# Optimization experiments

Measured on AMD Instinct MI355X. Metric: run time of the kernel, lower is better.

The kernel has to match this reference:

```python
import jax, jax.numpy as jnp
import numpy as np

B, S, D, H = 2, 2048, 2048, 16
HD = D // H  # 128


def setup_inputs() -> dict:
    key = jax.random.key(0)
    ks = jax.random.split(key, 6)
    sc = 0.02
    return {
        "x": jax.random.normal(ks[0], (B, S, D), jnp.float32),
        "attention_mask": jnp.ones((B, S), jnp.int32),
        "w_qkv": jax.random.normal(ks[1], (D, 3 * D), jnp.float32) * sc,
        "b_qkv": jnp.zeros((3 * D,), jnp.float32),
        "w_o": jax.random.normal(ks[2], (D, D), jnp.float32) * sc,
        "b_o": jnp.zeros((D,), jnp.float32),
        "ln1_w": jnp.ones((D,), jnp.float32),
        "w1": jax.random.normal(ks[3], (D, 8 * D), jnp.float32) * sc,
        "b1": jnp.zeros((8 * D,), jnp.float32),
        "w2": jax.random.normal(ks[4], (4 * D, D), jnp.float32) * sc,
        "b2": jnp.zeros((D,), jnp.float32),
        "ln2_w": jnp.ones((D,), jnp.float32),
    }


def rmsnorm(x, w, eps=1e-6):
    rms = jnp.sqrt(jnp.mean(x * x, axis=-1, keepdims=True) + eps)
    return w * (x / rms)


def rope_tables(seq_len, dim, base=10000.0):
    inv_freq = 1.0 / (base ** (jnp.arange(0, dim, 2, dtype=jnp.float32) / dim))
    t = jnp.arange(seq_len, dtype=jnp.float32)
    freqs = t[:, None] * inv_freq[None, :]          # [S, dim/2]
    emb = jnp.concatenate([freqs, freqs], axis=-1)  # [S, dim]
    return jnp.cos(emb), jnp.sin(emb)


def apply_rope(x, cos, sin):
    # Faithful to source: rotate pairs, then out = rot*cos + roll(rot,1)*sin
    xr = x.reshape(*x.shape[:-1], -1, 2)
    x1, x2 = xr[..., 0], xr[..., 1]
    rot = jnp.stack([-x2, x1], axis=-1).reshape(x.shape)
    return rot * cos + jnp.roll(rot, shift=1, axis=-1) * sin


def transformer_layer(x, attention_mask, w_qkv, b_qkv, w_o, b_o, ln1_w, w1, b1, w2, b2, ln2_w):
    residual = x
    qkv = x @ w_qkv + b_qkv                         # [B,S,3D]
    q, k, v = jnp.split(qkv, 3, axis=-1)
    split = lambda t: t.reshape(B, S, H, HD).transpose(0, 2, 1, 3)  # [B,H,S,HD]
    q, k, v = split(q), split(k), split(v)

    cos, sin = rope_tables(S, HD)                   # [S,HD], broadcasts over B,H
    q = apply_rope(q, cos, sin)
    k = apply_rope(k, cos, sin)

    scores = jnp.einsum("bhqd,bhkd->bhqk", q, k) / jnp.sqrt(jnp.float32(HD))
    mask = (attention_mask == 1)[:, None, None, :]  # [B,1,1,S]
    scores = jnp.where(mask, scores, -jnp.inf)
    attn = jax.nn.softmax(scores, axis=-1)
    out = jnp.einsum("bhqk,bhkd->bhqd", attn, v)
    out = out.transpose(0, 2, 1, 3).reshape(B, S, D)
    out = out @ w_o + b_o

    x = rmsnorm(out + residual, ln1_w)
    residual = x
    h = x @ w1 + b1                                 # [B,S,8D]
    h, gate = jnp.split(h, 2, axis=-1)
    h = h * jax.nn.gelu(gate, approximate=False)
    h = h @ w2 + b2
    return rmsnorm(h + residual, ln2_w)


def reference(x, attention_mask, w_qkv, b_qkv, w_o, b_o, ln1_w, w1, b1, w2, b2, ln2_w):
    return transformer_layer(x, attention_mask, w_qkv, b_qkv, w_o, b_o, ln1_w, w1, b1, w2, b2, ln2_w)
```

## Files before the change

### kernel.cpp

```cpp
#include <hip/hip_runtime.h>
#include <cstdint>
#include <cstring>

typedef unsigned short u16;
typedef __attribute__((ext_vector_type(8))) short short8;
typedef __attribute__((ext_vector_type(8))) unsigned short ushortx8;
typedef __attribute__((ext_vector_type(4))) float floatx4;

#define DEV __device__ __forceinline__

DEV u16 f2bf(float f) {
  union { float f; uint32_t u; } x; x.f = f;
  uint32_t r = x.u + 0x7fffu + ((x.u >> 16) & 1u);
  return (u16)(r >> 16);
}
DEV float bf2f(u16 h) {
  union { float f; uint32_t u; } x; x.u = ((uint32_t)h) << 16;
  return x.f;
}
DEV u16 f2h(float f) {
  union { u16 u; _Float16 h; } x; x.h = (_Float16)f; return x.u;
}
DEV float h2f(u16 h) {
  union { u16 u; _Float16 h; } x; x.u = h; return (float)x.h;
}
DEV float fexp2(float x) { return __builtin_amdgcn_exp2f(x); }
DEV float fast_gelu(float g) {
  float u = 0.7978845608f * (g + 0.044715f * g * g * g);
  float e = fexp2(-2.885390082f * fabsf(u));
  float th = (1.0f - e) / (1.0f + e);
  th = (u < 0.0f) ? -th : th;
  return 0.5f * g * (1.0f + th);
}
DEV void gload_lds16(const void* g, void* lds) {
  __builtin_amdgcn_global_load_lds(
      (const __attribute__((address_space(1))) char*)(uintptr_t)g,
      (__attribute__((address_space(3))) char*)(uintptr_t)lds, 16, 0, 0);
}


__global__ __launch_bounds__(256) void k_cvt_bf16(const float* __restrict__ in,
                                                  u16* __restrict__ out, int n) {
  int i = (blockIdx.x * 256 + threadIdx.x) * 8;
  if (i + 7 < n) {
    float4 a = *(const float4*)(in + i);
    float4 b = *(const float4*)(in + i + 4);
    ushortx8 o;
    o[0] = f2bf(a.x); o[1] = f2bf(a.y); o[2] = f2bf(a.z); o[3] = f2bf(a.w);
    o[4] = f2bf(b.x); o[5] = f2bf(b.y); o[6] = f2bf(b.z); o[7] = f2bf(b.w);
    *(ushortx8*)(out + i) = o;
  }
}

__global__ __launch_bounds__(256) void k_transpose_all(const float* __restrict__ Wq,
                                                       u16* __restrict__ WqT,
                                                       const float* __restrict__ Wo,
                                                       u16* __restrict__ WoT,
                                                       const float* __restrict__ W2,
                                                       u16* __restrict__ W2T) {
  __shared__ u16 t[64][70];
  int id = blockIdx.x;
  const float* W; u16* Wt; int R, C, tix;
  if (id < 3072)      { W = Wq; Wt = WqT; R = 2048; C = 6144; tix = id; }
  else if (id < 4096) { W = Wo; Wt = WoT; R = 2048; C = 2048; tix = id - 3072; }
  else                { W = W2; Wt = W2T; R = 8192; C = 2048; tix = id - 4096; }
  int ntc = C >> 6;
  int c0 = (tix % ntc) * 64, r0 = (tix / ntc) * 64;
  int cx = threadIdx.x & 15, ry = threadIdx.x >> 4;
#pragma unroll
  for (int i = 0; i < 4; ++i) {
    int row = ry + i * 16;
    float4 v = *(const float4*)(W + (size_t)(r0 + row) * C + c0 + cx * 4);
    ushort2 lo, hi;
    lo.x = f2bf(v.x); lo.y = f2bf(v.y);
    hi.x = f2bf(v.z); hi.y = f2bf(v.w);
    *(ushort2*)&t[row][cx * 4] = lo;
    *(ushort2*)&t[row][cx * 4 + 2] = hi;
  }
  __syncthreads();
#pragma unroll
  for (int i = 0; i < 4; ++i) {
    int col = ry + i * 16;
    ushort4 o;
    o.x = t[cx * 4 + 0][col]; o.y = t[cx * 4 + 1][col];
    o.z = t[cx * 4 + 2][col]; o.w = t[cx * 4 + 3][col];
    *(ushort4*)(Wt + (size_t)(c0 + col) * R + r0 + cx * 4) = o;
  }
}

__global__ __launch_bounds__(256) void k_transpose_w1p(const float* __restrict__ W,
                                                       u16* __restrict__ Wt) {
  __shared__ u16 t[64][70];
  int c0 = blockIdx.x * 64;
  int r0 = blockIdx.y * 64;
  int cx = threadIdx.x & 15, ry = threadIdx.x >> 4;
  int eta = c0 + cx * 4;
  int Bq = eta >> 8, ii = eta & 255, wn = (ii >> 6) & 3, rr = ii & 63, n = rr >> 4, tt = rr & 15;
  int src = Bq * 128 + wn * 32 + (n & 1) * 16 + tt + ((n >= 2) ? 8192 : 0);
#pragma unroll
  for (int i = 0; i < 4; ++i) {
    int row = ry + i * 16;
    float4 v = *(const float4*)(W + (size_t)(r0 + row) * 16384 + src);
    ushort2 lo, hi;
    lo.x = f2bf(v.x); lo.y = f2bf(v.y);
    hi.x = f2bf(v.z); hi.y = f2bf(v.w);
    *(ushort2*)&t[row][cx * 4] = lo;
    *(ushort2*)&t[row][cx * 4 + 2] = hi;
  }
  __syncthreads();
#pragma unroll
  for (int i = 0; i < 4; ++i) {
    ushort4 o;
    int col = ry + i * 16;
    o.x = t[cx * 4 + 0][col]; o.y = t[cx * 4 + 1][col];
    o.z = t[cx * 4 + 2][col]; o.w = t[cx * 4 + 3][col];
    *(ushort4*)(Wt + (size_t)(c0 + col) * 2048 + r0 + cx * 4) = o;
  }
}

__global__ __launch_bounds__(256) void k_rope_tab(float* __restrict__ ct, float* __restrict__ st) {
  int i = blockIdx.x * 256 + threadIdx.x;
  int s = i >> 6, j = i & 63;
  float invf = 1.0f / powf(10000.0f, (float)j * (1.0f / 64.0f));
  float ang = (float)s * invf;
  ct[i] = cosf(ang);
  st[i] = sinf(ang);
}

template <int EPI>
__global__ __launch_bounds__(512, 2) void k_gemm256(const u16* __restrict__ A,
                                                    const u16* __restrict__ Bt,
                                                    void* __restrict__ C,
                                                    const float* __restrict__ bias,
                                                    int M, int N, int K, int nsplit,
                                                    u16* __restrict__ qrO,
                                                    u16* __restrict__ krO,
                                                    u16* __restrict__ vtO,
                                                    const float* __restrict__ ctabO,
                                                    const float* __restrict__ stabO) {
  __shared__ __align__(16) u16 lds[4][2][8192];
  const int tid = threadIdx.x;
  const int w = tid >> 6, lane = tid & 63;
  const int l15 = lane & 15, l4 = lane >> 4;
  const int wm = w >> 2, wn = w & 3;
  const int nbn = N >> 8;
  const int nbm = M >> 8;

  int bm, bn, split = 0;
  if (nsplit == 1 && nbm == 16 && (nbn & 7) == 0) {
    const int xcd = blockIdx.x & 7, l = blockIdx.x >> 3;
    const int xr = xcd >> 1, xc = xcd & 1;
    const int stn = l >> 4, lbm = (l >> 2) & 3, lbn = l & 3;
    bm = xr * 4 + lbm;
    bn = xc * (nbn >> 1) + stn * 4 + lbn;
  } else {
    const int nwg = gridDim.x;
    const int q = nwg >> 3, r8 = nwg & 7;
    const int xcd = blockIdx.x & 7, loc = blockIdx.x >> 3;
    const int swz = (xcd < r8 ? xcd * (q + 1) : r8 * (q + 1) + (xcd - r8) * q) + loc;
    const int ntiles = nwg / nsplit;
    split = swz / ntiles;
    const int tix = swz % ntiles;
    bm = tix / nbn; bn = tix % nbn;
  }
  const int klen = K / nsplit;
  const int kofs = split * klen;

  const size_t abase = (size_t)bm * 256 * K + kofs;
  const size_t bbase = (size_t)bn * 256 * K + kofs;
  const int nt = klen >> 5;

  const int sr = tid >> 2;
  const int sc = (tid & 3) ^ ((sr >> 1) & 3);
  auto stage = [&](int kt, int li, int op) {
    const u16* src = op ? (Bt + bbase) : (A + abase);
    gload_lds16(src + (size_t)(li * 128 + sr) * K + kt * 32 + sc * 8,
                (void*)&lds[kt & 3][op][(li * 512 + w * 64) * 8]);
  };

  const int fro = l15 * 32 + (l4 ^ ((l15 >> 1) & 3)) * 8;

  floatx4 acc[8][4];
  floatx4 zero = {0.f, 0.f, 0.f, 0.f};
#pragma unroll
  for (int m = 0; m < 8; ++m)
#pragma unroll
    for (int n = 0; n < 4; ++n) acc[m][n] = zero;

  for (int kt = 0; kt < 3; ++kt)
    if (kt < nt) {
      stage(kt, 0, 0); stage(kt, 0, 1);
      stage(kt, 1, 0); stage(kt, 1, 1);
    }

  for (int t = 0; t < nt; ++t) {
    const int buf = t & 3;
    if (t < nt - 2)       asm volatile("s_waitcnt vmcnt(8)" ::: "memory");
    else if (t == nt - 2) asm volatile("s_waitcnt vmcnt(4)" ::: "memory");
    else                  asm volatile("s_waitcnt vmcnt(0)" ::: "memory");
    __builtin_amdgcn_sched_barrier(0);
    __builtin_amdgcn_s_barrier();
    const u16* Ab = &lds[buf][0][wm * 4096 + fro];
    const u16* Bb = &lds[buf][1][wn * 2048 + fro];
    short8 av[4], bv[4];
#pragma unroll
    for (int n = 0; n < 4; ++n) bv[n] = *(const short8*)(Bb + n * 512);
#pragma unroll
    for (int i = 0; i < 4; ++i) av[i] = *(const short8*)(Ab + i * 512);
    if (t + 3 < nt) { stage(t + 3, 0, 0); stage(t + 3, 0, 1); }
    asm volatile("s_waitcnt lgkmcnt(0)" ::: "memory");
    __builtin_amdgcn_sched_barrier(0);
    __builtin_amdgcn_s_setprio(1);
#pragma unroll
    for (int i = 0; i < 4; ++i)
#pragma unroll
      for (int n = 0; n < 4; ++n)
        acc[i][n] = __builtin_amdgcn_mfma_f32_16x16x32_bf16(av[i], bv[n], acc[i][n], 0, 0, 0);
    __builtin_amdgcn_s_setprio(0);
    __builtin_amdgcn_s_barrier();
#pragma unroll
    for (int i = 0; i < 4; ++i) av[i] = *(const short8*)(Ab + (4 + i) * 512);
    if (t + 3 < nt) { stage(t + 3, 1, 0); stage(t + 3, 1, 1); }
    asm volatile("s_waitcnt lgkmcnt(0)" ::: "memory");
    __builtin_amdgcn_sched_barrier(0);
    __builtin_amdgcn_s_setprio(1);
#pragma unroll
    for (int i = 0; i < 4; ++i)
#pragma unroll
      for (int n = 0; n < 4; ++n)
        acc[4 + i][n] = __builtin_amdgcn_mfma_f32_16x16x32_bf16(av[i], bv[n], acc[4 + i][n], 0, 0, 0);
    __builtin_amdgcn_s_setprio(0);
  }

  const int row0 = bm * 256 + wm * 128, col0 = bn * 256 + wn * 64;
  if (EPI == 2) {
    u16* P = (u16*)C + (size_t)split * M * N;
#pragma unroll
    for (int n = 0; n < 4; ++n) {
      int col = col0 + n * 16 + l15;
#pragma unroll
      for (int m = 0; m < 8; ++m)
#pragma unroll
        for (int j = 0; j < 4; ++j) {
          int row = row0 + m * 16 + l4 * 4 + j;
          P[(size_t)row * N + col] = f2h(acc[m][n][j]);
        }
    }
  } else if (EPI == 3) {
    __syncthreads();
    u16* ep = ((u16*)lds) + w * 4096;
    const int colA = bn * 128 + wn * 32;
#pragma unroll
    for (int n = 0; n < 2; ++n) {
      float ba = bias[colA + n * 16 + l15];
      float bg = bias[8192 + colA + n * 16 + l15];
#pragma unroll
      for (int m = 0; m < 8; ++m)
#pragma unroll
        for (int j = 0; j < 4; ++j) {
          float a = acc[m][n][j] + ba;
          float g = acc[m][n + 2][j] + bg;
          ep[(m * 16 + l4 * 4 + j) * 32 + n * 16 + l15] = f2bf(a * fast_gelu(g));
        }
    }
    const int rr = lane >> 2, cg = lane & 3;
    u16* Cg = (u16*)C;
    const int Nact = N >> 1;
#pragma unroll
    for (int pass = 0; pass < 8; ++pass) {
      short8 v = *(const short8*)&ep[(pass * 16 + rr) * 32 + cg * 8];
      size_t grow = row0 + pass * 16 + rr;
      *(short8*)&Cg[grow * Nact + colA + cg * 8] = v;
    }
  } else if (EPI == 4) {
    constexpr int PAD = 264;
    u16* T = (u16*)lds;
    const int bq = bm >> 3;
    const int srow0 = (bm & 7) * 256;
#pragma unroll 1
    for (int hf = 0; hf < 2; ++hf) {
      __syncthreads();
      if (wm == hf) {
#pragma unroll
        for (int n = 0; n < 4; ++n) {
          float bb = bias[bn * 256 + wn * 64 + n * 16 + l15];
#pragma unroll
          for (int m = 0; m < 8; ++m)
#pragma unroll
            for (int j = 0; j < 4; ++j)
              T[(m * 16 + l4 * 4 + j) * PAD + wn * 64 + n * 16 + l15] =
                  f2bf(acc[m][n][j] + bb);
        }
      }
      __syncthreads();
      if (bn < 16) {
        int sl = tid >> 2, hh = (tid >> 1) & 1, t2 = tid & 1;
        const u16* row = T + sl * PAD + hh * 128;
        int s = srow0 + hf * 128 + sl;
        int head = 2 * (bn & 7) + hh;
        u16* dst = (bn < 8 ? qrO : krO) +
                   (((size_t)bq * 16 + head) * 2048 + s) * 128 + t2 * 64;
        const float* ctr = ctabO + (s << 6);
        const float* str2 = stabO + (s << 6);
        const float qs = (bn < 8) ? 0.12751744f : 1.0f;
#pragma unroll
        for (int ch = 0; ch < 8; ++ch) {
          int d0 = t2 * 64 + ch * 8;
          ushortx8 xv = *(const ushortx8*)(row + d0);
          float xp = bf2f(row[(d0 + 126) & 127]);
          int f0 = d0 & 63;
          float4 c0v = *(const float4*)(ctr + f0);
          float4 c1v = *(const float4*)(ctr + f0 + 4);
          float4 s0v = *(const float4*)(str2 + f0);
          float4 s1v = *(const float4*)(str2 + f0 + 4);
          float cc[8] = {c0v.x, c0v.y, c0v.z, c0v.w, c1v.x, c1v.y, c1v.z, c1v.w};
          float sn[8] = {s0v.x, s0v.y, s0v.z, s0v.w, s1v.x, s1v.y, s1v.z, s1v.w};
          ushortx8 o;
#pragma unroll
          for (int pr = 0; pr < 4; ++pr) {
            float xe = bf2f((u16)xv[2 * pr]), xo = bf2f((u16)xv[2 * pr + 1]);
            o[2 * pr]     = f2bf((-xo * cc[2 * pr] + xp * sn[2 * pr]) * qs);
            o[2 * pr + 1] = f2bf(( xe * cc[2 * pr + 1] - xo * sn[2 * pr + 1]) * qs);
            xp = xe;
          }
          *(ushortx8*)(dst + ch * 8) = o;
        }
      } else {
        int hh = tid >> 8, dg = (tid >> 4) & 15, sc2 = tid & 15;
        int head = 2 * (bn - 16) + hh;
        int s0 = srow0 + hf * 128 + sc2 * 8;
        ushortx8 r[8];
#pragma unroll
        for (int i = 0; i < 8; ++i)
          r[i] = *(const ushortx8*)(T + (sc2 * 8 + i) * PAD + hh * 128 + dg * 8);
        u16* vbase = vtO + ((size_t)bq * 2048 + head * 128 + dg * 8) * 2048 + s0;
#pragma unroll
        for (int j2 = 0; j2 < 8; ++j2) {
          ushortx8 o;
#pragma unroll
          for (int i = 0; i < 8; ++i) o[i] = r[i][j2];
          *(ushortx8*)(vbase + (size_t)j2 * 2048) = o;
        }
      }
    }
  } else {
    __syncthreads();
    u16* ep = ((u16*)lds) + w * 8192;
#pragma unroll
    for (int n = 0; n < 4; ++n) {
      float bb = bias[col0 + n * 16 + l15];
#pragma unroll
      for (int m = 0; m < 8; ++m)
#pragma unroll
        for (int j = 0; j < 4; ++j)
          ep[(m * 16 + l4 * 4 + j) * 64 + n * 16 + l15] = f2bf(acc[m][n][j] + bb);
    }
    const int rr = lane >> 3, cg = lane & 7;
    u16* Cg = (u16*)C;
#pragma unroll
    for (int pass = 0; pass < 16; ++pass) {
      short8 v = *(const short8*)&ep[(pass * 8 + rr) * 64 + cg * 8];
      size_t grow = row0 + pass * 8 + rr;
      *(short8*)&Cg[grow * N + col0 + cg * 8] = v;
    }
  }
}

__global__ __launch_bounds__(512, 4) void k_attn(const u16* __restrict__ Qr,
                                                 const u16* __restrict__ Kr,
                                                 const u16* __restrict__ Vt,
                                                 const int* __restrict__ mask,
                                                 u16* __restrict__ O) {
  constexpr int S = 2048, HD = 128, H = 16;
  __shared__ __align__(16) u16 Ksh[64 * 128];
  __shared__ __align__(16) u16 Vsh[128 * 64];
  __shared__ __align__(16) u16 Psh[8][16 * 72];
  __shared__ float Msh[2048];

  const int bid = blockIdx.x;
  const int xcd = bid & 7, local = bid >> 3;
  const int bh = xcd * 4 + (local >> 4);
  const int qt = local & 15;
  const int b = bh >> 4, h = bh & 15;
  const int tid = threadIdx.x, wave = tid >> 6, lane = tid & 63;
  const int l15 = lane & 15, l4 = lane >> 4;
  const size_t bhs = (size_t)(b * H + h);
  const u16* Qb = Qr + bhs * S * HD;
  const u16* Kb = Kr + bhs * S * HD;
  const u16* Vb = Vt + bhs * HD * S;

  for (int i = tid; i < 2048; i += 512)
    Msh[i] = (mask[b * S + i] == 1) ? 0.0f : -1e30f;

  const int qrow = qt * 128 + wave * 16 + l15;
  short8 qf[4];
#pragma unroll
  for (int kk = 0; kk < 4; ++kk)
    qf[kk] = *(const short8*)&Qb[(size_t)qrow * HD + kk * 32 + l4 * 8];

  const int giA = tid, giB = 512 + tid;
  const int rKA = giA >> 4, gKA = giA & 15;
  const int rKB = giB >> 4, gKB = giB & 15;
  const int gsKA = (gKA & 8) | ((gKA ^ rKA) & 7);
  const int gsKB = (gKB & 8) | ((gKB ^ rKB) & 7);
  const int rVA = giA >> 3, gVA = giA & 7;
  const int rVB = giB >> 3, gVB = giB & 7;
  const int gsVA = (gVA ^ rVA) & 7;
  const int gsVB = (gVB ^ rVB) & 7;
  const u16* pKA = Kb + (size_t)rKA * HD + gsKA * 8;
  const u16* pKB = Kb + (size_t)rKB * HD + gsKB * 8;
  const u16* pVA = Vb + (size_t)rVA * S + gsVA * 8;
  const u16* pVB = Vb + (size_t)rVB * S + gsVB * 8;

  float m_run[4], l_run[4];
  floatx4 o_acc[8];
  floatx4 zero = {0.f, 0.f, 0.f, 0.f};
#pragma unroll
  for (int j = 0; j < 4; ++j) { m_run[j] = -1e30f; l_run[j] = 0.f; }
#pragma unroll
  for (int n = 0; n < 8; ++n) o_acc[n] = zero;

  uint4 k0 = *(const uint4*)pKA;
  uint4 k1 = *(const uint4*)pKB;
  uint4 v0 = *(const uint4*)pVA;
  uint4 v1 = *(const uint4*)pVB;

  for (int ktile = 0; ktile < S / 64; ++ktile) {
    __builtin_amdgcn_sched_barrier(0);
    __builtin_amdgcn_s_barrier();
    __builtin_amdgcn_sched_barrier(0);
    *(uint4*)&Ksh[(size_t)(0 * 512 + tid) * 8] = k0;
    *(uint4*)&Ksh[(size_t)(1 * 512 + tid) * 8] = k1;
    *(uint4*)&Vsh[(size_t)(0 * 512 + tid) * 8] = v0;
    *(uint4*)&Vsh[(size_t)(1 * 512 + tid) * 8] = v1;
    if (ktile + 1 < S / 64) {
      k0 = *(const uint4*)(pKA + (size_t)(ktile + 1) * 8192);
      k1 = *(const uint4*)(pKB + (size_t)(ktile + 1) * 8192);
      v0 = *(const uint4*)(pVA + (size_t)(ktile + 1) * 64);
      v1 = *(const uint4*)(pVB + (size_t)(ktile + 1) * 64);
    }
    asm volatile("s_waitcnt lgkmcnt(0)" ::: "memory");
    __builtin_amdgcn_sched_barrier(0);
    __builtin_amdgcn_s_barrier();
    __builtin_amdgcn_sched_barrier(0);

    floatx4 s_acc[4];
#pragma unroll
    for (int nf = 0; nf < 4; ++nf) s_acc[nf] = zero;
    __builtin_amdgcn_s_setprio(1);
#pragma unroll
    for (int kk = 0; kk < 4; ++kk) {
#pragma unroll
      for (int nf = 0; nf < 4; ++nf) {
        int key = nf * 16 + l15;
        int G = kk * 4 + l4;
        int lg = (G & 8) | ((G ^ key) & 7);
        short8 kv = *(const short8*)&Ksh[key * 128 + lg * 8];
        s_acc[nf] = __builtin_amdgcn_mfma_f32_16x16x32_bf16(qf[kk], kv, s_acc[nf], 0, 0, 0);
      }
    }
    __builtin_amdgcn_s_setprio(0);

    float p[4][4];
#pragma unroll
    for (int nf = 0; nf < 4; ++nf) {
      float ma = Msh[ktile * 64 + nf * 16 + l15];
#pragma unroll
      for (int j = 0; j < 4; ++j) p[nf][j] = s_acc[nf][j] + ma;
    }
#pragma unroll
    for (int j = 0; j < 4; ++j) {
      float mx = fmaxf(fmaxf(p[0][j], p[1][j]), fmaxf(p[2][j], p[3][j]));
      mx = fmaxf(mx, __shfl_xor(mx, 1));
      mx = fmaxf(mx, __shfl_xor(mx, 2));
      mx = fmaxf(mx, __shfl_xor(mx, 4));
      mx = fmaxf(mx, __shfl_xor(mx, 8));
      float mnew = fmaxf(m_run[j], mx);
      float corr = fexp2(m_run[j] - mnew);
      float ps = 0.f;
#pragma unroll
      for (int nf = 0; nf < 4; ++nf) {
        p[nf][j] = fexp2(p[nf][j] - mnew);
        ps += p[nf][j];
      }
      l_run[j] = l_run[j] * corr + ps;
      m_run[j] = mnew;
#pragma unroll
      for (int n = 0; n < 8; ++n) o_acc[n][j] *= corr;
    }

#pragma unroll
    for (int nf = 0; nf < 4; ++nf)
#pragma unroll
      for (int j = 0; j < 4; ++j)
        Psh[wave][(l4 * 4 + j) * 72 + nf * 16 + l15] = f2bf(p[nf][j]);

    __builtin_amdgcn_s_setprio(1);
#pragma unroll
    for (int ks = 0; ks < 2; ++ks) {
      short8 pa = *(const short8*)&Psh[wave][l15 * 72 + ks * 32 + l4 * 8];
#pragma unroll
      for (int nf2 = 0; nf2 < 8; ++nf2) {
        int hd = nf2 * 16 + l15;
        int G = ks * 4 + l4;
        short8 vv = *(const short8*)&Vsh[hd * 64 + ((G ^ hd) & 7) * 8];
        o_acc[nf2] = __builtin_amdgcn_mfma_f32_16x16x32_bf16(pa, vv, o_acc[nf2], 0, 0, 0);
      }
    }
    __builtin_amdgcn_s_setprio(0);
  }

#pragma unroll
  for (int j = 0; j < 4; ++j) {
    float ls = l_run[j];
    ls += __shfl_xor(ls, 1); ls += __shfl_xor(ls, 2);
    ls += __shfl_xor(ls, 4); ls += __shfl_xor(ls, 8);
    l_run[j] = ls;
  }

#pragma unroll
  for (int j = 0; j < 4; ++j) {
    float inv = 1.0f / l_run[j];
    int srow = qt * 128 + wave * 16 + l4 * 4 + j;
    size_t orow = ((size_t)b * S + srow) * 2048 + h * 128;
#pragma unroll
    for (int nf2 = 0; nf2 < 8; ++nf2)
      O[orow + nf2 * 16 + l15] = f2bf(o_acc[nf2][j] * inv);
  }
}

__global__ __launch_bounds__(256) void k_rms_fuse1(const u16* __restrict__ p0,
                                                   const u16* __restrict__ p1,
                                                   const float* __restrict__ bias,
                                                   const float* __restrict__ resid,
                                                   const float* __restrict__ w,
                                                   u16* __restrict__ ob) {
  int row = blockIdx.x;
  int t = threadIdx.x;
  size_t base = (size_t)row * 2048 + t * 8;
  ushortx8 a = *(const ushortx8*)(p0 + base);
  ushortx8 b = *(const ushortx8*)(p1 + base);
  float4 r0 = *(const float4*)(resid + base);
  float4 r1 = *(const float4*)(resid + base + 4);
  float4 c0 = *(const float4*)(bias + t * 8);
  float4 c1 = *(const float4*)(bias + t * 8 + 4);
  float rr[8] = {r0.x, r0.y, r0.z, r0.w, r1.x, r1.y, r1.z, r1.w};
  float cc[8] = {c0.x, c0.y, c0.z, c0.w, c1.x, c1.y, c1.z, c1.w};
  float v[8];
#pragma unroll
  for (int e = 0; e < 8; ++e)
    v[e] = h2f((u16)a[e]) + h2f((u16)b[e]) + rr[e] + cc[e];
  float ss = 0.f;
#pragma unroll
  for (int e = 0; e < 8; ++e) ss += v[e] * v[e];
#pragma unroll
  for (int d = 1; d < 64; d <<= 1) ss += __shfl_xor(ss, d);
  __shared__ float sred[4];
  if ((t & 63) == 0) sred[t >> 6] = ss;
  __syncthreads();
  float tot = sred[0] + sred[1] + sred[2] + sred[3];
  float scale = rsqrtf(tot * (1.0f / 2048.0f) + 1e-6f);
  const float* wp = w + t * 8;
  ushort4 q0, q1;
  q0.x = f2bf(v[0] * wp[0] * scale); q0.y = f2bf(v[1] * wp[1] * scale);
  q0.z = f2bf(v[2] * wp[2] * scale); q0.w = f2bf(v[3] * wp[3] * scale);
  q1.x = f2bf(v[4] * wp[4] * scale); q1.y = f2bf(v[5] * wp[5] * scale);
  q1.z = f2bf(v[6] * wp[6] * scale); q1.w = f2bf(v[7] * wp[7] * scale);
  *(ushort4*)(ob + base) = q0;
  *(ushort4*)(ob + base + 4) = q1;
}

__global__ __launch_bounds__(256) void k_rms_fuse2(const u16* __restrict__ p0,
                                                   const u16* __restrict__ p1,
                                                   const float* __restrict__ bias,
                                                   const u16* __restrict__ residb,
                                                   const float* __restrict__ w,
                                                   float* __restrict__ of) {
  int row = blockIdx.x;
  int t = threadIdx.x;
  size_t base = (size_t)row * 2048 + t * 8;
  ushortx8 a = *(const ushortx8*)(p0 + base);
  ushortx8 b = *(const ushortx8*)(p1 + base);
  ushortx8 rb = *(const ushortx8*)(residb + base);
  float4 c0 = *(const float4*)(bias + t * 8);
  float4 c1 = *(const float4*)(bias + t * 8 + 4);
  float cc[8] = {c0.x, c0.y, c0.z, c0.w, c1.x, c1.y, c1.z, c1.w};
  float v[8];
#pragma unroll
  for (int e = 0; e < 8; ++e)
    v[e] = h2f((u16)a[e]) + h2f((u16)b[e]) + bf2f((u16)rb[e]) + cc[e];
  float ss = 0.f;
#pragma unroll
  for (int e = 0; e < 8; ++e) ss += v[e] * v[e];
#pragma unroll
  for (int d = 1; d < 64; d <<= 1) ss += __shfl_xor(ss, d);
  __shared__ float sred[4];
  if ((t & 63) == 0) sred[t >> 6] = ss;
  __syncthreads();
  float tot = sred[0] + sred[1] + sred[2] + sred[3];
  float scale = rsqrtf(tot * (1.0f / 2048.0f) + 1e-6f);
  const float* wp = w + t * 8;
  float4 f0, f1;
  f0.x = v[0] * wp[0] * scale; f0.y = v[1] * wp[1] * scale;
  f0.z = v[2] * wp[2] * scale; f0.w = v[3] * wp[3] * scale;
  f1.x = v[4] * wp[4] * scale; f1.y = v[5] * wp[5] * scale;
  f1.z = v[6] * wp[6] * scale; f1.w = v[7] * wp[7] * scale;
  *(float4*)(of + base) = f0;
  *(float4*)(of + base + 4) = f1;
}

extern "C" void kernel_launch(void* const* d_in, const int* in_sizes, int n_in,
                              void* d_out, int out_size, void* d_ws, size_t ws_size,
                              hipStream_t stream) {
  const float* x     = (const float*)d_in[0];
  const int*   amask = (const int*)d_in[1];
  const float* w_qkv = (const float*)d_in[2];
  const float* b_qkv = (const float*)d_in[3];
  const float* w_o   = (const float*)d_in[4];
  const float* b_o   = (const float*)d_in[5];
  const float* ln1_w = (const float*)d_in[6];
  const float* w1    = (const float*)d_in[7];
  const float* b1    = (const float*)d_in[8];
  const float* w2    = (const float*)d_in[9];
  const float* b2    = (const float*)d_in[10];
  const float* ln2_w = (const float*)d_in[11];
  float* out = (float*)d_out;

  char* ws = (char*)d_ws;
  u16*   xb    = (u16*)(ws + 0);
  u16*   wqkvT = (u16*)(ws + 16777216);
  u16*   woT   = (u16*)(ws + 41943040);
  u16*   w1Tp  = (u16*)(ws + 50331648);
  u16*   w2T   = (u16*)(ws + 117440512);
  float* ctab  = (float*)(ws + 150994944);
  float* stab  = (float*)(ws + 151519232);
  u16*   qr    = (u16*)(ws + 202375168);
  u16*   kr    = (u16*)(ws + 219152384);
  u16*   vt    = (u16*)(ws + 235929600);
  u16*   aout  = (u16*)(ws + 252706816);
  u16*   x1b   = (u16*)(ws + 303038464);
  u16*   p01a  = (u16*)(ws + 152043520);
  u16*   act   = (u16*)(ws + 152043520);
  u16*   p01b  = (u16*)(ws + 219152384);

  k_cvt_bf16<<<4096, 256, 0, stream>>>(x, xb, 4096 * 2048);
  k_transpose_all<<<8192, 256, 0, stream>>>(w_qkv, wqkvT, w_o, woT, w2, w2T);
  k_transpose_w1p<<<dim3(256, 32), 256, 0, stream>>>(w1, w1Tp);
  k_rope_tab<<<512, 256, 0, stream>>>(ctab, stab);

  k_gemm256<4><<<16 * 24, 512, 0, stream>>>(xb, wqkvT, nullptr, b_qkv,
                                            4096, 6144, 2048, 1,
                                            qr, kr, vt, ctab, stab);
  k_attn<<<512, 512, 0, stream>>>(qr, kr, vt, amask, aout);

  k_gemm256<2><<<16 * 8 * 2, 512, 0, stream>>>(aout, woT, p01a, nullptr,
                                               4096, 2048, 2048, 2,
                                               nullptr, nullptr, nullptr, nullptr, nullptr);
  k_rms_fuse1<<<4096, 256, 0, stream>>>(p01a, p01a + (size_t)4096 * 2048, b_o, x, ln1_w, x1b);

  k_gemm256<3><<<16 * 64, 512, 0, stream>>>(x1b, w1Tp, act, b1,
                                            4096, 16384, 2048, 1,
                                            nullptr, nullptr, nullptr, nullptr, nullptr);

  k_gemm256<2><<<16 * 8 * 2, 512, 0, stream>>>(act, w2T, p01b, nullptr,
                                               4096, 2048, 8192, 2,
                                               nullptr, nullptr, nullptr, nullptr, nullptr);
  k_rms_fuse2<<<4096, 256, 0, stream>>>(p01b, p01b + (size_t)4096 * 2048, b2, x1b, ln2_w, out);
}
```

Baseline: 817.5 us.

## Add dedicated 128x256-tile QKV GEMM kernel with fused RoPE/V-transpose epilogue

Replaces the 256x256-tile QKV projection (384 workgroups) with a new 128x256-tile kernel launching 768 workgroups, using a 4-stage LDS pipeline, split MFMA phases with priority hints, and XCD-aware block mapping. The intent is better CU occupancy and wave balance for the 4096x6144 GEMM, which had too few tiles to fill the GPU evenly. The RoPE and V-transpose epilogue is carried over in single-pass form. The EPI==4 path is removed from the generic GEMM and its extra parameters dropped. Smaller tiles mean less operand reuse per tile and more global traffic.

```diff
diff --git a/kernel.cpp b/kernel.cpp
--- a/kernel.cpp
+++ b/kernel.cpp
@@ -127,17 +127,164 @@
   st[i] = sinf(ang);
 }
 
+__global__ __launch_bounds__(512, 1) void k_gemm128(const u16* __restrict__ A,
+                                                    const u16* __restrict__ Bt,
+                                                    const float* __restrict__ bias,
+                                                    u16* __restrict__ qrO,
+                                                    u16* __restrict__ krO,
+                                                    u16* __restrict__ vtO,
+                                                    const float* __restrict__ ctabO,
+                                                    const float* __restrict__ stabO) {
+  constexpr int K = 2048;
+  constexpr int nt = K / 32;
+  __shared__ __align__(16) u16 lds[4][12288];
+  const int tid = threadIdx.x;
+  const int w = tid >> 6, lane = tid & 63;
+  const int l15 = lane & 15, l4 = lane >> 4;
+  const int wm = w >> 2, wn = w & 3;
+  const int xcd = blockIdx.x & 7, loc = blockIdx.x >> 3;
+  const int swz = xcd * 96 + loc;
+  const int bm = swz / 24, bn = swz % 24;
+
+  const size_t abase = (size_t)bm * 128 * K;
+  const size_t bbase = (size_t)bn * 256 * K;
+
+  const int srA = tid >> 2;
+  const int scA = (tid & 3) ^ ((srA >> 1) & 3);
+  auto stageA = [&](int kt) {
+    gload_lds16(A + abase + (size_t)srA * K + kt * 32 + scA * 8,
+                (void*)&lds[kt & 3][(size_t)tid * 8]);
+  };
+  auto stageB = [&](int kt, int li) {
+    int g = li * 512 + tid;
+    int row = g >> 2;
+    int sc = (g & 3) ^ ((row >> 1) & 3);
+    gload_lds16(Bt + bbase + (size_t)row * K + kt * 32 + sc * 8,
+                (void*)&lds[kt & 3][4096 + (size_t)g * 8]);
+  };
+  const int fro = l15 * 32 + (l4 ^ ((l15 >> 1) & 3)) * 8;
+
+  floatx4 acc[4][4];
+  floatx4 zero = {0.f, 0.f, 0.f, 0.f};
+#pragma unroll
+  for (int m = 0; m < 4; ++m)
+#pragma unroll
+    for (int n = 0; n < 4; ++n) acc[m][n] = zero;
+
+  for (int kt = 0; kt < 3; ++kt) { stageA(kt); stageB(kt, 0); stageB(kt, 1); }
+
+  for (int t = 0; t < nt; ++t) {
+    const int buf = t & 3;
+    if (t < nt - 2)       asm volatile("s_waitcnt vmcnt(6)" ::: "memory");
+    else if (t == nt - 2) asm volatile("s_waitcnt vmcnt(3)" ::: "memory");
+    else                  asm volatile("s_waitcnt vmcnt(0)" ::: "memory");
+    __builtin_amdgcn_sched_barrier(0);
+    __builtin_amdgcn_s_barrier();
+    const u16* Ab = &lds[buf][wm * 2048 + fro];
+    const u16* Bb = &lds[buf][4096 + wn * 2048 + fro];
+    short8 av[4], bv[4];
+#pragma unroll
+    for (int n = 0; n < 4; ++n) bv[n] = *(const short8*)(Bb + n * 512);
+    av[0] = *(const short8*)(Ab);
+    av[1] = *(const short8*)(Ab + 512);
+    if (t + 3 < nt) { stageA(t + 3); stageB(t + 3, 0); }
+    asm volatile("s_waitcnt lgkmcnt(0)" ::: "memory");
+    __builtin_amdgcn_sched_barrier(0);
+    __builtin_amdgcn_s_setprio(1);
+#pragma unroll
+    for (int i = 0; i < 2; ++i)
+#pragma unroll
+      for (int n = 0; n < 4; ++n)
+        acc[i][n] = __builtin_amdgcn_mfma_f32_16x16x32_bf16(av[i], bv[n], acc[i][n], 0, 0, 0);
+    __builtin_amdgcn_s_setprio(0);
+    __builtin_amdgcn_s_barrier();
+    av[2] = *(const short8*)(Ab + 2 * 512);
+    av[3] = *(const short8*)(Ab + 3 * 512);
+    if (t + 3 < nt) stageB(t + 3, 1);
+    asm volatile("s_waitcnt lgkmcnt(0)" ::: "memory");
+    __builtin_amdgcn_sched_barrier(0);
+    __builtin_amdgcn_s_setprio(1);
+#pragma unroll
+    for (int i = 0; i < 2; ++i)
+#pragma unroll
+      for (int n = 0; n < 4; ++n)
+        acc[2 + i][n] = __builtin_amdgcn_mfma_f32_16x16x32_bf16(av[2 + i], bv[n], acc[2 + i][n], 0, 0, 0);
+    __builtin_amdgcn_s_setprio(0);
+  }
+
+  constexpr int PAD = 264;
+  u16* T = (u16*)lds;
+  __syncthreads();
+#pragma unroll
+  for (int n = 0; n < 4; ++n) {
+    float bb = bias[bn * 256 + wn * 64 + n * 16 + l15];
+#pragma unroll
+    for (int m = 0; m < 4; ++m)
+#pragma unroll
+      for (int j = 0; j < 4; ++j)
+        T[(wm * 64 + m * 16 + l4 * 4 + j) * PAD + wn * 64 + n * 16 + l15] =
+            f2bf(acc[m][n][j] + bb);
+  }
+  __syncthreads();
+  const int bq = bm >> 4;
+  const int srow0 = (bm & 15) * 128;
+  if (bn < 16) {
+    int sl = tid >> 2, hh = (tid >> 1) & 1, t2 = tid & 1;
+    const u16* row = T + sl * PAD + hh * 128;
+    int s = srow0 + sl;
+    int head = 2 * (bn & 7) + hh;
+    u16* dst = (bn < 8 ? qrO : krO) +
+               (((size_t)bq * 16 + head) * 2048 + s) * 128 + t2 * 64;
+    const float* ctr = ctabO + (s << 6);
+    const float* str2 = stabO + (s << 6);
+    const float qs = (bn < 8) ? 0.12751744f : 1.0f;
+#pragma unroll
+    for (int ch = 0; ch < 8; ++ch) {
+      int d0 = t2 * 64 + ch * 8;
+      ushortx8 xv = *(const ushortx8*)(row + d0);
+      float xp = bf2f(row[(d0 + 126) & 127]);
+      int f0 = d0 & 63;
+      float4 c0v = *(const float4*)(ctr + f0);
+      float4 c1v = *(const float4*)(ctr + f0 + 4);
+      float4 s0v = *(const float4*)(str2 + f0);
+      float4 s1v = *(const float4*)(str2 + f0 + 4);
+      float cc[8] = {c0v.x, c0v.y, c0v.z, c0v.w, c1v.x, c1v.y, c1v.z, c1v.w};
+      float sn[8] = {s0v.x, s0v.y, s0v.z, s0v.w, s1v.x, s1v.y, s1v.z, s1v.w};
+      ushortx8 o;
+#pragma unroll
+      for (int pr = 0; pr < 4; ++pr) {
+        float xe = bf2f((u16)xv[2 * pr]), xo = bf2f((u16)xv[2 * pr + 1]);
+        o[2 * pr]     = f2bf((-xo * cc[2 * pr] + xp * sn[2 * pr]) * qs);
+        o[2 * pr + 1] = f2bf(( xe * cc[2 * pr + 1] - xo * sn[2 * pr + 1]) * qs);
+        xp = xe;
+      }
+      *(ushortx8*)(dst + ch * 8) = o;
+    }
+  } else {
+    int hh = tid >> 8, dg = (tid >> 4) & 15, sc2 = tid & 15;
+    int head = 2 * (bn - 16) + hh;
+    int s0 = srow0 + sc2 * 8;
+    ushortx8 r[8];
+#pragma unroll
+    for (int i = 0; i < 8; ++i)
+      r[i] = *(const ushortx8*)(T + (sc2 * 8 + i) * PAD + hh * 128 + dg * 8);
+    u16* vbase = vtO + ((size_t)bq * 2048 + head * 128 + dg * 8) * 2048 + s0;
+#pragma unroll
+    for (int j2 = 0; j2 < 8; ++j2) {
+      ushortx8 o;
+#pragma unroll
+      for (int i = 0; i < 8; ++i) o[i] = r[i][j2];
+      *(ushortx8*)(vbase + (size_t)j2 * 2048) = o;
+    }
+  }
+}
+
 template <int EPI>
 __global__ __launch_bounds__(512, 2) void k_gemm256(const u16* __restrict__ A,
                                                     const u16* __restrict__ Bt,
                                                     void* __restrict__ C,
                                                     const float* __restrict__ bias,
-                                                    int M, int N, int K, int nsplit,
-                                                    u16* __restrict__ qrO,
-                                                    u16* __restrict__ krO,
-                                                    u16* __restrict__ vtO,
-                                                    const float* __restrict__ ctabO,
-                                                    const float* __restrict__ stabO) {
+                                                    int M, int N, int K, int nsplit) {
   __shared__ __align__(16) u16 lds[4][2][8192];
   const int tid = threadIdx.x;
   const int w = tid >> 6, lane = tid & 63;
@@ -271,77 +418,6 @@
       short8 v = *(const short8*)&ep[(pass * 16 + rr) * 32 + cg * 8];
       size_t grow = row0 + pass * 16 + rr;
       *(short8*)&Cg[grow * Nact + colA + cg * 8] = v;
-    }
-  } else if (EPI == 4) {
-    constexpr int PAD = 264;
-    u16* T = (u16*)lds;
-    const int bq = bm >> 3;
-    const int srow0 = (bm & 7) * 256;
-#pragma unroll 1
-    for (int hf = 0; hf < 2; ++hf) {
-      __syncthreads();
-      if (wm == hf) {
-#pragma unroll
-        for (int n = 0; n < 4; ++n) {
-          float bb = bias[bn * 256 + wn * 64 + n * 16 + l15];
-#pragma unroll
-          for (int m = 0; m < 8; ++m)
-#pragma unroll
-            for (int j = 0; j < 4; ++j)
-              T[(m * 16 + l4 * 4 + j) * PAD + wn * 64 + n * 16 + l15] =
-                  f2bf(acc[m][n][j] + bb);
-        }
-      }
-      __syncthreads();
-      if (bn < 16) {
-        int sl = tid >> 2, hh = (tid >> 1) & 1, t2 = tid & 1;
-        const u16* row = T + sl * PAD + hh * 128;
-        int s = srow0 + hf * 128 + sl;
-        int head = 2 * (bn & 7) + hh;
-        u16* dst = (bn < 8 ? qrO : krO) +
-                   (((size_t)bq * 16 + head) * 2048 + s) * 128 + t2 * 64;
-        const float* ctr = ctabO + (s << 6);
-        const float* str2 = stabO + (s << 6);
-        const float qs = (bn < 8) ? 0.12751744f : 1.0f;
-#pragma unroll
-        for (int ch = 0; ch < 8; ++ch) {
-          int d0 = t2 * 64 + ch * 8;
-          ushortx8 xv = *(const ushortx8*)(row + d0);
-          float xp = bf2f(row[(d0 + 126) & 127]);
-          int f0 = d0 & 63;
-          float4 c0v = *(const float4*)(ctr + f0);
-          float4 c1v = *(const float4*)(ctr + f0 + 4);
-          float4 s0v = *(const float4*)(str2 + f0);
-          float4 s1v = *(const float4*)(str2 + f0 + 4);
-          float cc[8] = {c0v.x, c0v.y, c0v.z, c0v.w, c1v.x, c1v.y, c1v.z, c1v.w};
-          float sn[8] = {s0v.x, s0v.y, s0v.z, s0v.w, s1v.x, s1v.y, s1v.z, s1v.w};
-          ushortx8 o;
-#pragma unroll
-          for (int pr = 0; pr < 4; ++pr) {
-            float xe = bf2f((u16)xv[2 * pr]), xo = bf2f((u16)xv[2 * pr + 1]);
-            o[2 * pr]     = f2bf((-xo * cc[2 * pr] + xp * sn[2 * pr]) * qs);
-            o[2 * pr + 1] = f2bf(( xe * cc[2 * pr + 1] - xo * sn[2 * pr + 1]) * qs);
-            xp = xe;
-          }
-          *(ushortx8*)(dst + ch * 8) = o;
-        }
-      } else {
-        int hh = tid >> 8, dg = (tid >> 4) & 15, sc2 = tid & 15;
-        int head = 2 * (bn - 16) + hh;
-        int s0 = srow0 + hf * 128 + sc2 * 8;
-        ushortx8 r[8];
-#pragma unroll
-        for (int i = 0; i < 8; ++i)
-          r[i] = *(const ushortx8*)(T + (sc2 * 8 + i) * PAD + hh * 128 + dg * 8);
-        u16* vbase = vtO + ((size_t)bq * 2048 + head * 128 + dg * 8) * 2048 + s0;
-#pragma unroll
-        for (int j2 = 0; j2 < 8; ++j2) {
-          ushortx8 o;
-#pragma unroll
-          for (int i = 0; i < 8; ++i) o[i] = r[i][j2];
-          *(ushortx8*)(vbase + (size_t)j2 * 2048) = o;
-        }
-      }
     }
   } else {
     __syncthreads();
@@ -648,22 +724,17 @@
   k_transpose_w1p<<<dim3(256, 32), 256, 0, stream>>>(w1, w1Tp);
   k_rope_tab<<<512, 256, 0, stream>>>(ctab, stab);
 
-  k_gemm256<4><<<16 * 24, 512, 0, stream>>>(xb, wqkvT, nullptr, b_qkv,
-                                            4096, 6144, 2048, 1,
-                                            qr, kr, vt, ctab, stab);
+  k_gemm128<<<768, 512, 0, stream>>>(xb, wqkvT, b_qkv, qr, kr, vt, ctab, stab);
   k_attn<<<512, 512, 0, stream>>>(qr, kr, vt, amask, aout);
 
   k_gemm256<2><<<16 * 8 * 2, 512, 0, stream>>>(aout, woT, p01a, nullptr,
-                                               4096, 2048, 2048, 2,
-                                               nullptr, nullptr, nullptr, nullptr, nullptr);
+                                               4096, 2048, 2048, 2);
   k_rms_fuse1<<<4096, 256, 0, stream>>>(p01a, p01a + (size_t)4096 * 2048, b_o, x, ln1_w, x1b);
 
   k_gemm256<3><<<16 * 64, 512, 0, stream>>>(x1b, w1Tp, act, b1,
-                                            4096, 16384, 2048, 1,
-                                            nullptr, nullptr, nullptr, nullptr, nullptr);
+                                            4096, 16384, 2048, 1);
 
   k_gemm256<2><<<16 * 8 * 2, 512, 0, stream>>>(act, w2T, p01b, nullptr,
-                                               4096, 2048, 8192, 2,
-                                               nullptr, nullptr, nullptr, nullptr, nullptr);
+                                               4096, 2048, 8192, 2);
   k_rms_fuse2<<<4096, 256, 0, stream>>>(p01b, p01b + (size_t)4096 * 2048, b2, x1b, ln2_w, out);
 }
```

Result: no change. 819.3 us (+0.2%).
